# Kernel optimization log

Hardware: AMD Instinct MI355X
Metric: run time of the kernel (lower is better)

## Reference

```python
import jax, jax.numpy as jnp
import numpy as np
from jax import lax

B, N, T, D, H = 8, 64, 128, 256, 8
DK = D // H
K_SIZE = 3
SCALE = 1.0 / np.sqrt(DK)
NEG = -1e9


def conv1d_same(x, w, b):
    # x: (M, Cin, T), w: (Cout, Cin, K) torch Conv1d layout, padding='same'
    y = lax.conv_general_dilated(x, w, window_strides=(1,), padding='SAME',
                                 dimension_numbers=('NCH', 'OIH', 'NCH'))
    return y + b[None, :, None]


def setup_inputs() -> dict:
    rng = jax.random.key(0)
    ks = jax.random.split(rng, 12)
    s = 0.05
    return {
        'query': jax.random.normal(ks[0], (B, N, T, D), jnp.float32),
        'key': jax.random.normal(ks[1], (B, N, T, D), jnp.float32),
        'value': jax.random.normal(ks[2], (B, N, T, D), jnp.float32),
        'key_padding_mask': jax.random.randint(ks[3], (B, N, T), 0, 2).astype(jnp.bool_),
        'attn_mask': jax.random.randint(ks[4], (T, T), 0, 2).astype(jnp.int32),
        'conv_q_w': jax.random.normal(ks[5], (D, D, K_SIZE), jnp.float32) * s,
        'conv_q_b': jnp.zeros((D,), jnp.float32),
        'conv_k_w': jax.random.normal(ks[6], (D, D, K_SIZE), jnp.float32) * s,
        'conv_k_b': jnp.zeros((D,), jnp.float32),
        'v_w': jax.random.normal(ks[7], (D, D), jnp.float32) * s,  # torch Linear: (out, in)
        'v_b': jnp.zeros((D,), jnp.float32),
        'out_w': jax.random.normal(ks[8], (D, D), jnp.float32) * s,
        'out_b': jnp.zeros((D,), jnp.float32),
    }


def reference(query, key, value, key_padding_mask, attn_mask,
              conv_q_w, conv_q_b, conv_k_w, conv_k_b, v_w, v_b, out_w, out_b):
    Bq, Nq, Tq, Dq = query.shape
    Tk = key.shape[2]
    # Conv1d Q/K projections ('same' padding, mode='1d')
    q_in = query.reshape(Bq * Nq, Tq, Dq).transpose(0, 2, 1)  # (BN, D, Tq)
    k_in = key.reshape(Bq * Nq, Tk, Dq).transpose(0, 2, 1)
    q = conv1d_same(q_in, conv_q_w, conv_q_b).transpose(0, 2, 1)  # (BN, Tq, D)
    k = conv1d_same(k_in, conv_k_w, conv_k_b).transpose(0, 2, 1)
    Q = q.reshape(Bq, Nq, Tq, H, DK).transpose(0, 1, 3, 2, 4)  # (B,N,H,Tq,dk)
    Kh = k.reshape(Bq, Nq, Tk, H, DK).transpose(0, 1, 3, 2, 4)
    V = (jnp.einsum('bntd,ed->bnte', value, v_w) + v_b)
    V = V.reshape(Bq, Nq, Tk, H, DK).transpose(0, 1, 3, 2, 4)  # (B,N,H,Tk,dk)
    scores = jnp.einsum('bnhqd,bnhkd->bnhqk', Q, Kh) * SCALE
    scores = jnp.where(key_padding_mask[:, :, None, None, :], NEG, scores)
    scores = jnp.where(attn_mask[None, None, None, :, :] == 0, NEG, scores)
    attn = jax.nn.softmax(scores, axis=-1)
    x = jnp.einsum('bnhqk,bnhkd->bnhqd', attn, V)
    x = x.transpose(0, 1, 3, 2, 4).reshape(Bq, Nq, Tq, Dq)
    return jnp.einsum('bntd,ed->bnte', x, out_w) + out_b
```

## Files before the change

kernel.cpp:

```cpp
#include <hip/hip_runtime.h>

#define TT 128
#define DD 256
#define NH 8
#define HD 32
#define SCALEF 0.17677669529663687f
#define NEGV -1e9f

typedef short bf16x8 __attribute__((ext_vector_type(8)));
typedef float f32x4 __attribute__((ext_vector_type(4)));

__device__ inline unsigned short f2bf(float f) {
    unsigned u = __float_as_uint(f);
    unsigned r = (u + 0x7FFFu + ((u >> 16) & 1u)) >> 16;
    return (unsigned short)r;
}
__device__ inline unsigned pk2(float a, float b) {
    return (unsigned)f2bf(a) | ((unsigned)f2bf(b) << 16);
}

__global__ void cvt_weights_kernel(
    const float* __restrict__ wq, const float* __restrict__ wk,
    const float* __restrict__ vw, const float* __restrict__ ow,
    const unsigned char* __restrict__ kpm8,
    unsigned short* __restrict__ wqf, unsigned short* __restrict__ wkf,
    unsigned short* __restrict__ vwf, unsigned short* __restrict__ owf,
    int* __restrict__ flagp)
{
    if (blockIdx.x == 1280) {
        __shared__ int f;
        if (threadIdx.x == 0) f = 0;
        __syncthreads();
        bool loc = false;
        for (int i = threadIdx.x; i < 4096; i += 256)
            if ((i & 3) && kpm8[i]) loc = true;
        if (loc) f = 1;
        __syncthreads();
        if (threadIdx.x == 0) *flagp = f;
        return;
    }
    int t = blockIdx.x * 256 + threadIdx.x;
    if (t < 196608) {
        int f = t >> 9, r = t & 511, l = r >> 3, s = r & 7;
        int k = f >> 7, jr = (f >> 3) & 15, c32 = f & 7;
        int j = jr * 16 + (l & 15);
        int ci = c32 * 32 + (l >> 4) * 8 + s;
        int src = j * 768 + ci * 3 + k;
        wqf[t] = f2bf(wq[src]);
        wkf[t] = f2bf(wk[src]);
    } else {
        int o = t - 196608;
        int oo = o & 65535;
        int f = oo >> 9, r = oo & 511, l = r >> 3, s = r & 7;
        int er = f >> 3, c32 = f & 7;
        int e = er * 16 + (l & 15);
        int d = c32 * 32 + (l >> 4) * 8 + s;
        if (o < 65536) vwf[oo] = f2bf(vw[e * 256 + d]);
        else           owf[oo] = f2bf(ow[e * 256 + d]);
    }
}

#define XP 264

__global__ __launch_bounds__(512, 4) void proj_kernel(
    const float* __restrict__ query, const float* __restrict__ key,
    const float* __restrict__ value,
    const unsigned short* __restrict__ wqf, const unsigned short* __restrict__ wkf,
    const unsigned short* __restrict__ vwf,
    const float* __restrict__ bq, const float* __restrict__ bk,
    const float* __restrict__ vbias,
    short* __restrict__ qkb, short* __restrict__ vbuf)
{
    __shared__ __align__(16) short Xs[130 * XP];

    const int tid = threadIdx.x;
    const int bn = blockIdx.x, which = blockIdx.y;
    const int lane = tid & 63, wv = tid >> 6;
    const int lr = lane & 15, rg = lane >> 4, k8 = rg * 8;

    const float* __restrict__ X =
        (which == 0 ? query : which == 1 ? key : value) + (size_t)bn * TT * DD;

    if (which < 2) {
        const unsigned short* __restrict__ W = which ? wkf : wqf;
        const float* __restrict__ bias = which ? bk : bq;
        const int j0 = (wv & 3) * 64;
        const int t0 = (wv >> 2) * 64;

        for (int i = tid; i < 130 * 64; i += 512) {
            int row = i >> 6, c4 = i & 63, g = row - 1;
            float4 x4 = make_float4(0.f, 0.f, 0.f, 0.f);
            if (g >= 0 && g < TT)
                x4 = *(const float4*)(X + g * DD + c4 * 4);
            uint2 p; p.x = pk2(x4.x, x4.y); p.y = pk2(x4.z, x4.w);
            *(uint2*)&Xs[row * XP + c4 * 4] = p;
        }
        __syncthreads();

        f32x4 acc[4][4];
        #pragma unroll
        for (int mf = 0; mf < 4; ++mf)
            #pragma unroll
            for (int r = 0; r < 4; ++r) {
                float bv = bias[j0 + mf * 16 + rg * 4 + r];
                #pragma unroll
                for (int nf = 0; nf < 4; ++nf) acc[mf][nf][r] = bv;
            }

        #pragma unroll
        for (int k = 0; k < 3; ++k) {
            #pragma unroll
            for (int c32 = 0; c32 < 8; ++c32) {
                bf16x8 aa[4];
                #pragma unroll
                for (int mf = 0; mf < 4; ++mf)
                    aa[mf] = *(const bf16x8*)(W +
                        ((((k * 16 + (j0 >> 4) + mf) * 8 + c32) << 9)
                         + lane * 8));
                bf16x8 bb[4];
                #pragma unroll
                for (int nf = 0; nf < 4; ++nf)
                    bb[nf] = *(const bf16x8*)&Xs[(t0 + nf * 16 + lr + k) * XP
                                                 + c32 * 32 + k8];
                #pragma unroll
                for (int mf = 0; mf < 4; ++mf)
                    #pragma unroll
                    for (int nf = 0; nf < 4; ++nf)
                        acc[mf][nf] = __builtin_amdgcn_mfma_f32_16x16x32_bf16(
                            aa[mf], bb[nf], acc[mf][nf], 0, 0, 0);
            }
        }
        short* cell = qkb + (size_t)bn * 65536 + which * 32768;
        #pragma unroll
        for (int mf = 0; mf < 4; ++mf)
            #pragma unroll
            for (int nf = 0; nf < 4; ++nf) {
                int fr = ((t0 >> 4) + nf) * 8 + (j0 >> 5) + (mf >> 1);
                int off = (fr << 9) + (lr + 16 * ((mf & 1) * 2 + (rg >> 1))) * 8
                          + (rg & 1) * 4;
                uint2 p;
                p.x = pk2(acc[mf][nf][0], acc[mf][nf][1]);
                p.y = pk2(acc[mf][nf][2], acc[mf][nf][3]);
                *(uint2*)&cell[off] = p;
            }
    } else {
        const int e0 = (wv & 3) * 64;
        const int t0 = (wv >> 2) * 64;

        for (int i = tid; i < 128 * 64; i += 512) {
            int row = i >> 6, c4 = i & 63;
            float4 x4 = *(const float4*)(X + row * DD + c4 * 4);
            uint2 p; p.x = pk2(x4.x, x4.y); p.y = pk2(x4.z, x4.w);
            *(uint2*)&Xs[row * XP + c4 * 4] = p;
        }
        __syncthreads();

        f32x4 acc4[4][4];
        #pragma unroll
        for (int nf = 0; nf < 4; ++nf) {
            float bv = vbias[e0 + nf * 16 + lr];
            #pragma unroll
            for (int mf = 0; mf < 4; ++mf)
                #pragma unroll
                for (int r = 0; r < 4; ++r) acc4[mf][nf][r] = bv;
        }

        #pragma unroll
        for (int c32 = 0; c32 < 8; ++c32) {
            bf16x8 aa[4];
            #pragma unroll
            for (int mf = 0; mf < 4; ++mf)
                aa[mf] = *(const bf16x8*)&Xs[(t0 + mf * 16 + lr) * XP
                                             + c32 * 32 + k8];
            bf16x8 bb[4];
            #pragma unroll
            for (int nf = 0; nf < 4; ++nf)
                bb[nf] = *(const bf16x8*)(vwf +
                    (((((e0 >> 4) + nf) * 8 + c32) << 9) + lane * 8));
            #pragma unroll
            for (int mf = 0; mf < 4; ++mf)
                #pragma unroll
                for (int nf = 0; nf < 4; ++nf)
                    acc4[mf][nf] = __builtin_amdgcn_mfma_f32_16x16x32_bf16(
                        aa[mf], bb[nf], acc4[mf][nf], 0, 0, 0);
        }
        short* vcell = vbuf + (size_t)bn * 32768;
        #pragma unroll
        for (int mf = 0; mf < 4; ++mf)
            #pragma unroll
            for (int nf = 0; nf < 4; ++nf) {
                int fr = (((e0 >> 4) + nf) << 2) + (t0 >> 5) + (mf >> 1);
                int off = (fr << 9) + (lr + 16 * ((mf & 1) * 2 + (rg >> 1))) * 8
                          + (rg & 1) * 4;
                uint2 p;
                p.x = pk2(acc4[mf][nf][0], acc4[mf][nf][1]);
                p.y = pk2(acc4[mf][nf][2], acc4[mf][nf][3]);
                *(uint2*)&vcell[off] = p;
            }
    }
}

__global__ __launch_bounds__(256, 3) void attn_kernel(
    short* __restrict__ qkb, const short* __restrict__ vbuf,
    const unsigned char* __restrict__ kpm8, const int* __restrict__ kpm32,
    const int* __restrict__ amask, const int* __restrict__ flagp)
{
    __shared__ __align__(16) short Ps[4 * 32 * 136];
    __shared__ __align__(16) short xl[128 * 40];
    __shared__ unsigned char maskb[2048];

    const int tid = threadIdx.x;
    int bid = blockIdx.x;
    int bnh = (bid & 7) * 512 + (bid >> 3);
    const int bn = bnh >> 3, h = bnh & 7;

    const int lane = tid & 63, wv = tid >> 6;
    const int lr = lane & 15, rg = lane >> 4, k8 = rg * 8;
    const int m0 = wv * 32;
    const bool kpm_u8 = (*flagp != 0);

    {
        const unsigned char* kp8 = kpm8 + (size_t)bn * TT;
        const int* kp32 = kpm32 + (size_t)bn * TT;
        for (int i = tid; i < 2048; i += 256) {
            int row = i >> 4, c = i & 15;
            unsigned m = 0;
            #pragma unroll
            for (int nf = 0; nf < 8; ++nf) {
                int col = c + nf * 16;
                int kdead = kpm_u8 ? (int)kp8[col] : kp32[col];
                int adead = (amask[row * TT + col] == 0) ? 1 : 0;
                m |= (unsigned)(((kdead != 0) ? 1 : 0) | adead) << nf;
            }
            maskb[i] = (unsigned char)m;
        }
    }

    const short* qcell = qkb + (size_t)bn * 65536;
    short* kcell = qkb + (size_t)bn * 65536 + 32768;

    bf16x8 qa[2];
    #pragma unroll
    for (int mf = 0; mf < 2; ++mf)
        qa[mf] = *(const bf16x8*)(qcell + ((((wv * 2 + mf) * 8 + h) << 9)
                                           + lane * 8));
    bf16x8 kb[8];
    #pragma unroll
    for (int nf = 0; nf < 8; ++nf)
        kb[nf] = *(const bf16x8*)(kcell + (((nf * 8 + h) << 9) + lane * 8));

    __syncthreads();

    f32x4 sc[2][8];
    #pragma unroll
    for (int nf = 0; nf < 8; ++nf) {
        f32x4 z = { 0.f, 0.f, 0.f, 0.f };
        sc[0][nf] = __builtin_amdgcn_mfma_f32_16x16x32_bf16(qa[0], kb[nf], z, 0, 0, 0);
        sc[1][nf] = __builtin_amdgcn_mfma_f32_16x16x32_bf16(qa[1], kb[nf], z, 0, 0, 0);
    }

    float linv[2][4];
    #pragma unroll
    for (int mf = 0; mf < 2; ++mf)
        #pragma unroll
        for (int r = 0; r < 4; ++r) {
            int row = m0 + mf * 16 + rg * 4 + r;
            unsigned mb = maskb[row * 16 + lr];
            float v[8];
            float vmax = -3.4e38f;
            #pragma unroll
            for (int nf = 0; nf < 8; ++nf) {
                float t = sc[mf][nf][r] * SCALEF;
                if ((mb >> nf) & 1) t = NEGV;
                v[nf] = t;
                vmax = fmaxf(vmax, t);
            }
            #pragma unroll
            for (int d = 1; d < 16; d <<= 1)
                vmax = fmaxf(vmax, __shfl_xor(vmax, d, 64));
            float ls = 0.f;
            #pragma unroll
            for (int nf = 0; nf < 8; ++nf) {
                float p = __expf(v[nf] - vmax);
                ls += p;
                sc[mf][nf][r] = p;
            }
            #pragma unroll
            for (int d = 1; d < 16; d <<= 1)
                ls += __shfl_xor(ls, d, 64);
            linv[mf][r] = 1.f / ls;
        }

    short* Pw = Ps + wv * 32 * 136;
    #pragma unroll
    for (int mf = 0; mf < 2; ++mf)
        #pragma unroll
        for (int r = 0; r < 4; ++r) {
            int q = mf * 16 + rg * 4 + r;
            #pragma unroll
            for (int nf = 0; nf < 8; ++nf)
                Pw[q * 136 + nf * 16 + lr] = (short)f2bf(sc[mf][nf][r]);
        }

    f32x4 xacc[2][2];
    {
        f32x4 z = { 0.f, 0.f, 0.f, 0.f };
        xacc[0][0] = z; xacc[0][1] = z; xacc[1][0] = z; xacc[1][1] = z;
    }
    const short* vcell = vbuf + (size_t)bn * 32768;
    #pragma unroll
    for (int kk = 0; kk < 4; ++kk) {
        bf16x8 pa0 = *(const bf16x8*)&Pw[(lr) * 136 + kk * 32 + k8];
        bf16x8 pa1 = *(const bf16x8*)&Pw[(16 + lr) * 136 + kk * 32 + k8];
        bf16x8 vb0 = *(const bf16x8*)(vcell + ((((h * 2 + 0) * 4 + kk) << 9) + lane * 8));
        bf16x8 vb1 = *(const bf16x8*)(vcell + ((((h * 2 + 1) * 4 + kk) << 9) + lane * 8));
        xacc[0][0] = __builtin_amdgcn_mfma_f32_16x16x32_bf16(pa0, vb0, xacc[0][0], 0, 0, 0);
        xacc[0][1] = __builtin_amdgcn_mfma_f32_16x16x32_bf16(pa0, vb1, xacc[0][1], 0, 0, 0);
        xacc[1][0] = __builtin_amdgcn_mfma_f32_16x16x32_bf16(pa1, vb0, xacc[1][0], 0, 0, 0);
        xacc[1][1] = __builtin_amdgcn_mfma_f32_16x16x32_bf16(pa1, vb1, xacc[1][1], 0, 0, 0);
    }

    __syncthreads();

    #pragma unroll
    for (int mf = 0; mf < 2; ++mf)
        #pragma unroll
        for (int nf = 0; nf < 2; ++nf)
            #pragma unroll
            for (int r = 0; r < 4; ++r) {
                int t = m0 + mf * 16 + rg * 4 + r;
                xl[t * 40 + nf * 16 + lr] =
                    (short)f2bf(xacc[mf][nf][r] * linv[mf][r]);
            }
    __syncthreads();

    #pragma unroll
    for (int p = 0; p < 2; ++p) {
        int idx = tid + p * 256;
        int f = idx >> 6, l = idx & 63;
        int row = f * 16 + (l & 15), c8 = (l >> 4) * 8;
        uint4 v = *(const uint4*)&xl[row * 40 + c8];
        *(uint4*)(kcell + (((f * 8 + h) << 9) + l * 8)) = v;
    }
}

__global__ __launch_bounds__(256, 2) void out_proj_mfma(
    short* __restrict__ qkb, const unsigned short* __restrict__ owf,
    const float* __restrict__ ob)
{
    const int tid = threadIdx.x;
    const int lane = tid & 63, wv = tid >> 6;
    const int lr = lane & 15, rg = lane >> 4;
    const int m0 = wv * 32;
    const short* xf = qkb + (size_t)blockIdx.x * 65536 + 32768;
    float* fcell = (float*)qkb + (size_t)blockIdx.x * 32768;

    f32x4 acc[2][16];
    {
        f32x4 z = { 0.f, 0.f, 0.f, 0.f };
        #pragma unroll
        for (int nf = 0; nf < 16; ++nf) { acc[0][nf] = z; acc[1][nf] = z; }
    }

    #pragma unroll
    for (int dc = 0; dc < 8; ++dc) {
        bf16x8 a0 = *(const bf16x8*)(xf + ((((wv * 2 + 0) * 8 + dc) << 9) + lane * 8));
        bf16x8 a1 = *(const bf16x8*)(xf + ((((wv * 2 + 1) * 8 + dc) << 9) + lane * 8));
        #pragma unroll
        for (int nf = 0; nf < 16; ++nf) {
            bf16x8 b = *(const bf16x8*)(owf + (((nf * 8 + dc) << 9) + lane * 8));
            acc[0][nf] = __builtin_amdgcn_mfma_f32_16x16x32_bf16(a0, b, acc[0][nf], 0, 0, 0);
            acc[1][nf] = __builtin_amdgcn_mfma_f32_16x16x32_bf16(a1, b, acc[1][nf], 0, 0, 0);
        }
    }

    #pragma unroll
    for (int mf = 0; mf < 2; ++mf)
        #pragma unroll
        for (int nf = 0; nf < 16; ++nf) {
            float bb = ob[nf * 16 + lr];
            #pragma unroll
            for (int r = 0; r < 4; ++r)
                fcell[(m0 + mf * 16 + rg * 4 + r) * DD + nf * 16 + lr] =
                    acc[mf][nf][r] + bb;
        }
}

extern "C" void kernel_launch(void* const* d_in, const int* in_sizes, int n_in,
                              void* d_out, int out_size, void* d_ws, size_t ws_size,
                              hipStream_t stream) {
    (void)in_sizes; (void)n_in; (void)out_size; (void)ws_size;
    const float* query = (const float*)d_in[0];
    const float* key   = (const float*)d_in[1];
    const float* value = (const float*)d_in[2];
    const void*  kpm   = d_in[3];
    const int*   amask = (const int*)d_in[4];
    const float* wq = (const float*)d_in[5];
    const float* bq = (const float*)d_in[6];
    const float* wk = (const float*)d_in[7];
    const float* bk = (const float*)d_in[8];
    const float* vw = (const float*)d_in[9];
    const float* vb = (const float*)d_in[10];
    const float* ow = (const float*)d_in[11];
    const float* ob = (const float*)d_in[12];

    short* qkb = (short*)d_out;
    unsigned short* wqf = (unsigned short*)d_ws;
    unsigned short* wkf = wqf + 196608;
    unsigned short* vwf = wkf + 196608;
    unsigned short* owf = vwf + 65536;
    int* flagp = (int*)((short*)d_ws + 524288);
    short* vbuf = (short*)d_ws + 524296;

    cvt_weights_kernel<<<dim3(1281), dim3(256), 0, stream>>>(
        wq, wk, vw, ow, (const unsigned char*)kpm, wqf, wkf, vwf, owf, flagp);

    proj_kernel<<<dim3(512, 3), dim3(512), 0, stream>>>(
        query, key, value, wqf, wkf, vwf, bq, bk, vb, qkb, vbuf);

    attn_kernel<<<dim3(4096), dim3(256), 0, stream>>>(
        qkb, vbuf, (const unsigned char*)kpm, (const int*)kpm, amask, flagp);

    out_proj_mfma<<<dim3(512), dim3(256), 0, stream>>>(qkb, owf, ob);
}
```

Measured before the change: 199.4 us.

## Fuse V projection into attention kernel with one block per (b,n)

Moves the value linear projection out of proj_kernel and into a new fused kernel that computes V for one (b,n) slice into shared memory. The same block then runs attention for all 8 heads, one wave per head, iterating over four 32-row query tiles. This removes the global V buffer write and re-read and drops the attention grid from 4096 small blocks to 512 larger ones. In exchange it uses a large shared-memory footprint (about 150KB), which lowers occupancy, and it serialises the query tiles within each wave.

```diff
diff --git a/kernel.cpp b/kernel.cpp
--- a/kernel.cpp
+++ b/kernel.cpp
@@ -64,12 +64,9 @@
 
 __global__ __launch_bounds__(512, 4) void proj_kernel(
     const float* __restrict__ query, const float* __restrict__ key,
-    const float* __restrict__ value,
     const unsigned short* __restrict__ wqf, const unsigned short* __restrict__ wkf,
-    const unsigned short* __restrict__ vwf,
     const float* __restrict__ bq, const float* __restrict__ bk,
-    const float* __restrict__ vbias,
-    short* __restrict__ qkb, short* __restrict__ vbuf)
+    short* __restrict__ qkb)
 {
     __shared__ __align__(16) short Xs[130 * XP];
 
@@ -79,150 +76,99 @@
     const int lr = lane & 15, rg = lane >> 4, k8 = rg * 8;
 
     const float* __restrict__ X =
-        (which == 0 ? query : which == 1 ? key : value) + (size_t)bn * TT * DD;
-
-    if (which < 2) {
-        const unsigned short* __restrict__ W = which ? wkf : wqf;
-        const float* __restrict__ bias = which ? bk : bq;
-        const int j0 = (wv & 3) * 64;
-        const int t0 = (wv >> 2) * 64;
-
-        for (int i = tid; i < 130 * 64; i += 512) {
-            int row = i >> 6, c4 = i & 63, g = row - 1;
-            float4 x4 = make_float4(0.f, 0.f, 0.f, 0.f);
-            if (g >= 0 && g < TT)
-                x4 = *(const float4*)(X + g * DD + c4 * 4);
-            uint2 p; p.x = pk2(x4.x, x4.y); p.y = pk2(x4.z, x4.w);
-            *(uint2*)&Xs[row * XP + c4 * 4] = p;
-        }
-        __syncthreads();
-
-        f32x4 acc[4][4];
-        #pragma unroll
-        for (int mf = 0; mf < 4; ++mf)
-            #pragma unroll
-            for (int r = 0; r < 4; ++r) {
-                float bv = bias[j0 + mf * 16 + rg * 4 + r];
-                #pragma unroll
-                for (int nf = 0; nf < 4; ++nf) acc[mf][nf][r] = bv;
-            }
-
-        #pragma unroll
-        for (int k = 0; k < 3; ++k) {
-            #pragma unroll
-            for (int c32 = 0; c32 < 8; ++c32) {
-                bf16x8 aa[4];
-                #pragma unroll
-                for (int mf = 0; mf < 4; ++mf)
-                    aa[mf] = *(const bf16x8*)(W +
-                        ((((k * 16 + (j0 >> 4) + mf) * 8 + c32) << 9)
-                         + lane * 8));
-                bf16x8 bb[4];
-                #pragma unroll
-                for (int nf = 0; nf < 4; ++nf)
-                    bb[nf] = *(const bf16x8*)&Xs[(t0 + nf * 16 + lr + k) * XP
-                                                 + c32 * 32 + k8];
-                #pragma unroll
-                for (int mf = 0; mf < 4; ++mf)
-                    #pragma unroll
-                    for (int nf = 0; nf < 4; ++nf)
-                        acc[mf][nf] = __builtin_amdgcn_mfma_f32_16x16x32_bf16(
-                            aa[mf], bb[nf], acc[mf][nf], 0, 0, 0);
-            }
-        }
-        short* cell = qkb + (size_t)bn * 65536 + which * 32768;
-        #pragma unroll
-        for (int mf = 0; mf < 4; ++mf)
-            #pragma unroll
-            for (int nf = 0; nf < 4; ++nf) {
-                int fr = ((t0 >> 4) + nf) * 8 + (j0 >> 5) + (mf >> 1);
-                int off = (fr << 9) + (lr + 16 * ((mf & 1) * 2 + (rg >> 1))) * 8
-                          + (rg & 1) * 4;
-                uint2 p;
-                p.x = pk2(acc[mf][nf][0], acc[mf][nf][1]);
-                p.y = pk2(acc[mf][nf][2], acc[mf][nf][3]);
-                *(uint2*)&cell[off] = p;
-            }
-    } else {
-        const int e0 = (wv & 3) * 64;
-        const int t0 = (wv >> 2) * 64;
-
-        for (int i = tid; i < 128 * 64; i += 512) {
-            int row = i >> 6, c4 = i & 63;
-            float4 x4 = *(const float4*)(X + row * DD + c4 * 4);
-            uint2 p; p.x = pk2(x4.x, x4.y); p.y = pk2(x4.z, x4.w);
-            *(uint2*)&Xs[row * XP + c4 * 4] = p;
-        }
-        __syncthreads();
-
-        f32x4 acc4[4][4];
-        #pragma unroll
-        for (int nf = 0; nf < 4; ++nf) {
-            float bv = vbias[e0 + nf * 16 + lr];
-            #pragma unroll
-            for (int mf = 0; mf < 4; ++mf)
-                #pragma unroll
-                for (int r = 0; r < 4; ++r) acc4[mf][nf][r] = bv;
-        }
-
+        (which == 0 ? query : key) + (size_t)bn * TT * DD;
+    const unsigned short* __restrict__ W = which ? wkf : wqf;
+    const float* __restrict__ bias = which ? bk : bq;
+    const int j0 = (wv & 3) * 64;
+    const int t0 = (wv >> 2) * 64;
+
+    for (int i = tid; i < 130 * 64; i += 512) {
+        int row = i >> 6, c4 = i & 63, g = row - 1;
+        float4 x4 = make_float4(0.f, 0.f, 0.f, 0.f);
+        if (g >= 0 && g < TT)
+            x4 = *(const float4*)(X + g * DD + c4 * 4);
+        uint2 p; p.x = pk2(x4.x, x4.y); p.y = pk2(x4.z, x4.w);
+        *(uint2*)&Xs[row * XP + c4 * 4] = p;
+    }
+    __syncthreads();
+
+    f32x4 acc[4][4];
+    #pragma unroll
+    for (int mf = 0; mf < 4; ++mf)
+        #pragma unroll
+        for (int r = 0; r < 4; ++r) {
+            float bv = bias[j0 + mf * 16 + rg * 4 + r];
+            #pragma unroll
+            for (int nf = 0; nf < 4; ++nf) acc[mf][nf][r] = bv;
+        }
+
+    #pragma unroll
+    for (int k = 0; k < 3; ++k) {
         #pragma unroll
         for (int c32 = 0; c32 < 8; ++c32) {
             bf16x8 aa[4];
             #pragma unroll
             for (int mf = 0; mf < 4; ++mf)
-                aa[mf] = *(const bf16x8*)&Xs[(t0 + mf * 16 + lr) * XP
+                aa[mf] = *(const bf16x8*)(W +
+                    ((((k * 16 + (j0 >> 4) + mf) * 8 + c32) << 9)
+                     + lane * 8));
+            bf16x8 bb[4];
+            #pragma unroll
+            for (int nf = 0; nf < 4; ++nf)
+                bb[nf] = *(const bf16x8*)&Xs[(t0 + nf * 16 + lr + k) * XP
                                              + c32 * 32 + k8];
-            bf16x8 bb[4];
-            #pragma unroll
-            for (int nf = 0; nf < 4; ++nf)
-                bb[nf] = *(const bf16x8*)(vwf +
-                    (((((e0 >> 4) + nf) * 8 + c32) << 9) + lane * 8));
             #pragma unroll
             for (int mf = 0; mf < 4; ++mf)
                 #pragma unroll
                 for (int nf = 0; nf < 4; ++nf)
-                    acc4[mf][nf] = __builtin_amdgcn_mfma_f32_16x16x32_bf16(
-                        aa[mf], bb[nf], acc4[mf][nf], 0, 0, 0);
-        }
-        short* vcell = vbuf + (size_t)bn * 32768;
-        #pragma unroll
-        for (int mf = 0; mf < 4; ++mf)
-            #pragma unroll
-            for (int nf = 0; nf < 4; ++nf) {
-                int fr = (((e0 >> 4) + nf) << 2) + (t0 >> 5) + (mf >> 1);
-                int off = (fr << 9) + (lr + 16 * ((mf & 1) * 2 + (rg >> 1))) * 8
-                          + (rg & 1) * 4;
-                uint2 p;
-                p.x = pk2(acc4[mf][nf][0], acc4[mf][nf][1]);
-                p.y = pk2(acc4[mf][nf][2], acc4[mf][nf][3]);
-                *(uint2*)&vcell[off] = p;
-            }
-    }
-}
-
-__global__ __launch_bounds__(256, 3) void attn_kernel(
-    short* __restrict__ qkb, const short* __restrict__ vbuf,
+                    acc[mf][nf] = __builtin_amdgcn_mfma_f32_16x16x32_bf16(
+                        aa[mf], bb[nf], acc[mf][nf], 0, 0, 0);
+        }
+    }
+    short* cell = qkb + (size_t)bn * 65536 + which * 32768;
+    #pragma unroll
+    for (int mf = 0; mf < 4; ++mf)
+        #pragma unroll
+        for (int nf = 0; nf < 4; ++nf) {
+            int fr = ((t0 >> 4) + nf) * 8 + (j0 >> 5) + (mf >> 1);
+            int off = (fr << 9) + (lr + 16 * ((mf & 1) * 2 + (rg >> 1))) * 8
+                      + (rg & 1) * 4;
+            uint2 p;
+            p.x = pk2(acc[mf][nf][0], acc[mf][nf][1]);
+            p.y = pk2(acc[mf][nf][2], acc[mf][nf][3]);
+            *(uint2*)&cell[off] = p;
+        }
+}
+
+__global__ __launch_bounds__(512, 2) void vproj_attn_fused(
+    short* qkb, const float* __restrict__ value,
+    const unsigned short* __restrict__ vwf, const float* __restrict__ vbias,
     const unsigned char* __restrict__ kpm8, const int* __restrict__ kpm32,
     const int* __restrict__ amask, const int* __restrict__ flagp)
 {
-    __shared__ __align__(16) short Ps[4 * 32 * 136];
-    __shared__ __align__(16) short xl[128 * 40];
+    __shared__ __align__(16) short U[34816];
+    __shared__ __align__(16) short VsT[32768];
+    __shared__ __align__(16) short xlw[8 * 32 * 40];
     __shared__ unsigned char maskb[2048];
 
     const int tid = threadIdx.x;
-    int bid = blockIdx.x;
-    int bnh = (bid & 7) * 512 + (bid >> 3);
-    const int bn = bnh >> 3, h = bnh & 7;
-
+    const int bid = blockIdx.x;
+    const int bn = (bid & 7) * 64 + (bid >> 3);
     const int lane = tid & 63, wv = tid >> 6;
     const int lr = lane & 15, rg = lane >> 4, k8 = rg * 8;
-    const int m0 = wv * 32;
     const bool kpm_u8 = (*flagp != 0);
 
     {
+        const float* __restrict__ Xv = value + (size_t)bn * TT * DD;
+        for (int i = tid; i < 128 * 64; i += 512) {
+            int row = i >> 6, c4 = i & 63;
+            float4 x4 = *(const float4*)(Xv + row * DD + c4 * 4);
+            uint2 p; p.x = pk2(x4.x, x4.y); p.y = pk2(x4.z, x4.w);
+            *(uint2*)&U[row * XP + c4 * 4] = p;
+        }
         const unsigned char* kp8 = kpm8 + (size_t)bn * TT;
         const int* kp32 = kpm32 + (size_t)bn * TT;
-        for (int i = tid; i < 2048; i += 256) {
+        for (int i = tid; i < 2048; i += 512) {
             int row = i >> 4, c = i & 15;
             unsigned m = 0;
             #pragma unroll
@@ -235,112 +181,154 @@
             maskb[i] = (unsigned char)m;
         }
     }
+    __syncthreads();
+
+    {
+        f32x4 vacc[8][2];
+        #pragma unroll
+        for (int nf = 0; nf < 2; ++nf) {
+            float bv = vbias[wv * HD + nf * 16 + lr];
+            #pragma unroll
+            for (int mf = 0; mf < 8; ++mf)
+                #pragma unroll
+                for (int r = 0; r < 4; ++r) vacc[mf][nf][r] = bv;
+        }
+        #pragma unroll
+        for (int c32 = 0; c32 < 8; ++c32) {
+            bf16x8 bb[2];
+            #pragma unroll
+            for (int nf = 0; nf < 2; ++nf)
+                bb[nf] = *(const bf16x8*)(vwf +
+                    ((((wv * 2 + nf) * 8 + c32) << 9) + lane * 8));
+            bf16x8 aa[8];
+            #pragma unroll
+            for (int mf = 0; mf < 8; ++mf)
+                aa[mf] = *(const bf16x8*)&U[(mf * 16 + lr) * XP
+                                            + c32 * 32 + k8];
+            #pragma unroll
+            for (int mf = 0; mf < 8; ++mf)
+                #pragma unroll
+                for (int nf = 0; nf < 2; ++nf)
+                    vacc[mf][nf] = __builtin_amdgcn_mfma_f32_16x16x32_bf16(
+                        aa[mf], bb[nf], vacc[mf][nf], 0, 0, 0);
+        }
+        #pragma unroll
+        for (int mf = 0; mf < 8; ++mf)
+            #pragma unroll
+            for (int nf = 0; nf < 2; ++nf) {
+                int fr = (wv * 2 + nf) * 4 + (mf >> 1);
+                int off = (fr << 9) + (lr + 16 * ((mf & 1) * 2 + (rg >> 1))) * 8
+                          + (rg & 1) * 4;
+                uint2 p;
+                p.x = pk2(vacc[mf][nf][0], vacc[mf][nf][1]);
+                p.y = pk2(vacc[mf][nf][2], vacc[mf][nf][3]);
+                *(uint2*)&VsT[off] = p;
+            }
+    }
+    __syncthreads();
 
     const short* qcell = qkb + (size_t)bn * 65536;
     short* kcell = qkb + (size_t)bn * 65536 + 32768;
 
-    bf16x8 qa[2];
-    #pragma unroll
-    for (int mf = 0; mf < 2; ++mf)
-        qa[mf] = *(const bf16x8*)(qcell + ((((wv * 2 + mf) * 8 + h) << 9)
-                                           + lane * 8));
     bf16x8 kb[8];
     #pragma unroll
     for (int nf = 0; nf < 8; ++nf)
-        kb[nf] = *(const bf16x8*)(kcell + (((nf * 8 + h) << 9) + lane * 8));
-
-    __syncthreads();
-
-    f32x4 sc[2][8];
-    #pragma unroll
-    for (int nf = 0; nf < 8; ++nf) {
-        f32x4 z = { 0.f, 0.f, 0.f, 0.f };
-        sc[0][nf] = __builtin_amdgcn_mfma_f32_16x16x32_bf16(qa[0], kb[nf], z, 0, 0, 0);
-        sc[1][nf] = __builtin_amdgcn_mfma_f32_16x16x32_bf16(qa[1], kb[nf], z, 0, 0, 0);
-    }
-
-    float linv[2][4];
-    #pragma unroll
-    for (int mf = 0; mf < 2; ++mf)
-        #pragma unroll
-        for (int r = 0; r < 4; ++r) {
-            int row = m0 + mf * 16 + rg * 4 + r;
-            unsigned mb = maskb[row * 16 + lr];
-            float v[8];
-            float vmax = -3.4e38f;
-            #pragma unroll
-            for (int nf = 0; nf < 8; ++nf) {
-                float t = sc[mf][nf][r] * SCALEF;
-                if ((mb >> nf) & 1) t = NEGV;
-                v[nf] = t;
-                vmax = fmaxf(vmax, t);
+        kb[nf] = *(const bf16x8*)(kcell + (((nf * 8 + wv) << 9) + lane * 8));
+
+    short* Pw = U + wv * 32 * 136;
+    short* xw = xlw + wv * 32 * 40;
+
+    #pragma unroll
+    for (int mtp = 0; mtp < 4; ++mtp) {
+        bf16x8 qa[2];
+        #pragma unroll
+        for (int mf = 0; mf < 2; ++mf)
+            qa[mf] = *(const bf16x8*)(qcell +
+                ((((mtp * 2 + mf) * 8 + wv) << 9) + lane * 8));
+
+        f32x4 sc[2][8];
+        #pragma unroll
+        for (int nf = 0; nf < 8; ++nf) {
+            f32x4 z = { 0.f, 0.f, 0.f, 0.f };
+            sc[0][nf] = __builtin_amdgcn_mfma_f32_16x16x32_bf16(qa[0], kb[nf], z, 0, 0, 0);
+            sc[1][nf] = __builtin_amdgcn_mfma_f32_16x16x32_bf16(qa[1], kb[nf], z, 0, 0, 0);
+        }
+
+        float linv[2][4];
+        #pragma unroll
+        for (int mf = 0; mf < 2; ++mf)
+            #pragma unroll
+            for (int r = 0; r < 4; ++r) {
+                int row = mtp * 32 + mf * 16 + rg * 4 + r;
+                unsigned mb = maskb[row * 16 + lr];
+                float v[8];
+                float vmax = -3.4e38f;
+                #pragma unroll
+                for (int nf = 0; nf < 8; ++nf) {
+                    float t = sc[mf][nf][r] * SCALEF;
+                    if ((mb >> nf) & 1) t = NEGV;
+                    v[nf] = t;
+                    vmax = fmaxf(vmax, t);
+                }
+                #pragma unroll
+                for (int d = 1; d < 16; d <<= 1)
+                    vmax = fmaxf(vmax, __shfl_xor(vmax, d, 64));
+                float ls = 0.f;
+                #pragma unroll
+                for (int nf = 0; nf < 8; ++nf) {
+                    float p = __expf(v[nf] - vmax);
+                    ls += p;
+                    sc[mf][nf][r] = p;
+                }
+                #pragma unroll
+                for (int d = 1; d < 16; d <<= 1)
+                    ls += __shfl_xor(ls, d, 64);
+                linv[mf][r] = 1.f / ls;
             }
-            #pragma unroll
-            for (int d = 1; d < 16; d <<= 1)
-                vmax = fmaxf(vmax, __shfl_xor(vmax, d, 64));
-            float ls = 0.f;
-            #pragma unroll
-            for (int nf = 0; nf < 8; ++nf) {
-                float p = __expf(v[nf] - vmax);
-                ls += p;
-                sc[mf][nf][r] = p;
+
+        #pragma unroll
+        for (int mf = 0; mf < 2; ++mf)
+            #pragma unroll
+            for (int r = 0; r < 4; ++r) {
+                int q = mf * 16 + rg * 4 + r;
+                #pragma unroll
+                for (int nf = 0; nf < 8; ++nf)
+                    Pw[q * 136 + nf * 16 + lr] = (short)f2bf(sc[mf][nf][r]);
             }
-            #pragma unroll
-            for (int d = 1; d < 16; d <<= 1)
-                ls += __shfl_xor(ls, d, 64);
-            linv[mf][r] = 1.f / ls;
-        }
-
-    short* Pw = Ps + wv * 32 * 136;
-    #pragma unroll
-    for (int mf = 0; mf < 2; ++mf)
-        #pragma unroll
-        for (int r = 0; r < 4; ++r) {
-            int q = mf * 16 + rg * 4 + r;
-            #pragma unroll
-            for (int nf = 0; nf < 8; ++nf)
-                Pw[q * 136 + nf * 16 + lr] = (short)f2bf(sc[mf][nf][r]);
-        }
-
-    f32x4 xacc[2][2];
-    {
-        f32x4 z = { 0.f, 0.f, 0.f, 0.f };
-        xacc[0][0] = z; xacc[0][1] = z; xacc[1][0] = z; xacc[1][1] = z;
-    }
-    const short* vcell = vbuf + (size_t)bn * 32768;
-    #pragma unroll
-    for (int kk = 0; kk < 4; ++kk) {
-        bf16x8 pa0 = *(const bf16x8*)&Pw[(lr) * 136 + kk * 32 + k8];
-        bf16x8 pa1 = *(const bf16x8*)&Pw[(16 + lr) * 136 + kk * 32 + k8];
-        bf16x8 vb0 = *(const bf16x8*)(vcell + ((((h * 2 + 0) * 4 + kk) << 9) + lane * 8));
-        bf16x8 vb1 = *(const bf16x8*)(vcell + ((((h * 2 + 1) * 4 + kk) << 9) + lane * 8));
-        xacc[0][0] = __builtin_amdgcn_mfma_f32_16x16x32_bf16(pa0, vb0, xacc[0][0], 0, 0, 0);
-        xacc[0][1] = __builtin_amdgcn_mfma_f32_16x16x32_bf16(pa0, vb1, xacc[0][1], 0, 0, 0);
-        xacc[1][0] = __builtin_amdgcn_mfma_f32_16x16x32_bf16(pa1, vb0, xacc[1][0], 0, 0, 0);
-        xacc[1][1] = __builtin_amdgcn_mfma_f32_16x16x32_bf16(pa1, vb1, xacc[1][1], 0, 0, 0);
-    }
-
-    __syncthreads();
-
-    #pragma unroll
-    for (int mf = 0; mf < 2; ++mf)
-        #pragma unroll
-        for (int nf = 0; nf < 2; ++nf)
-            #pragma unroll
-            for (int r = 0; r < 4; ++r) {
-                int t = m0 + mf * 16 + rg * 4 + r;
-                xl[t * 40 + nf * 16 + lr] =
-                    (short)f2bf(xacc[mf][nf][r] * linv[mf][r]);
-            }
-    __syncthreads();
-
-    #pragma unroll
-    for (int p = 0; p < 2; ++p) {
-        int idx = tid + p * 256;
-        int f = idx >> 6, l = idx & 63;
-        int row = f * 16 + (l & 15), c8 = (l >> 4) * 8;
-        uint4 v = *(const uint4*)&xl[row * 40 + c8];
-        *(uint4*)(kcell + (((f * 8 + h) << 9) + l * 8)) = v;
+
+        f32x4 xacc[2][2];
+        {
+            f32x4 z = { 0.f, 0.f, 0.f, 0.f };
+            xacc[0][0] = z; xacc[0][1] = z; xacc[1][0] = z; xacc[1][1] = z;
+        }
+        #pragma unroll
+        for (int kk = 0; kk < 4; ++kk) {
+            bf16x8 pa0 = *(const bf16x8*)&Pw[lr * 136 + kk * 32 + k8];
+            bf16x8 pa1 = *(const bf16x8*)&Pw[(16 + lr) * 136 + kk * 32 + k8];
+            bf16x8 vb0 = *(const bf16x8*)&VsT[(((wv * 2 + 0) * 4 + kk) << 9) + lane * 8];
+            bf16x8 vb1 = *(const bf16x8*)&VsT[(((wv * 2 + 1) * 4 + kk) << 9) + lane * 8];
+            xacc[0][0] = __builtin_amdgcn_mfma_f32_16x16x32_bf16(pa0, vb0, xacc[0][0], 0, 0, 0);
+            xacc[0][1] = __builtin_amdgcn_mfma_f32_16x16x32_bf16(pa0, vb1, xacc[0][1], 0, 0, 0);
+            xacc[1][0] = __builtin_amdgcn_mfma_f32_16x16x32_bf16(pa1, vb0, xacc[1][0], 0, 0, 0);
+            xacc[1][1] = __builtin_amdgcn_mfma_f32_16x16x32_bf16(pa1, vb1, xacc[1][1], 0, 0, 0);
+        }
+
+        #pragma unroll
+        for (int mf = 0; mf < 2; ++mf)
+            #pragma unroll
+            for (int nf = 0; nf < 2; ++nf)
+                #pragma unroll
+                for (int r = 0; r < 4; ++r)
+                    xw[(mf * 16 + rg * 4 + r) * 40 + nf * 16 + lr] =
+                        (short)f2bf(xacc[mf][nf][r] * linv[mf][r]);
+
+        #pragma unroll
+        for (int mf = 0; mf < 2; ++mf) {
+            int fr = (mtp * 2 + mf) * 8 + wv;
+            uint4 v = *(const uint4*)&xw[(mf * 16 + (lane & 15)) * 40
+                                         + (lane >> 4) * 8];
+            *(uint4*)(kcell + (fr << 9) + lane * 8) = v;
+        }
     }
 }
 
@@ -410,16 +398,16 @@
     unsigned short* vwf = wkf + 196608;
     unsigned short* owf = vwf + 65536;
     int* flagp = (int*)((short*)d_ws + 524288);
-    short* vbuf = (short*)d_ws + 524296;
 
     cvt_weights_kernel<<<dim3(1281), dim3(256), 0, stream>>>(
         wq, wk, vw, ow, (const unsigned char*)kpm, wqf, wkf, vwf, owf, flagp);
 
-    proj_kernel<<<dim3(512, 3), dim3(512), 0, stream>>>(
-        query, key, value, wqf, wkf, vwf, bq, bk, vb, qkb, vbuf);
-
-    attn_kernel<<<dim3(4096), dim3(256), 0, stream>>>(
-        qkb, vbuf, (const unsigned char*)kpm, (const int*)kpm, amask, flagp);
+    proj_kernel<<<dim3(512, 2), dim3(512), 0, stream>>>(
+        query, key, wqf, wkf, bq, bk, qkb);
+
+    vproj_attn_fused<<<dim3(512), dim3(512), 0, stream>>>(
+        qkb, value, vwf, vb, (const unsigned char*)kpm, (const int*)kpm,
+        amask, flagp);
 
     out_proj_mfma<<<dim3(512), dim3(256), 0, stream>>>(qkb, owf, ob);
 }
```

Result: faster. 179.7 us (-9.8%).
